# Kernel optimization log

Measured on AMD Instinct MI355X. Metric: run time of the kernel, lower is better.

## Reference

```python
import jax, jax.numpy as jnp
import numpy as np

B, L, XS, YS, A, C, NL = 32, 4096, 256, 256, 4, 64, 5  # batch, seq, x_size, y_size, n_actions, hid_cnn, cnn_layers


def _conv2d(x, w):
    # x: [N,Cin,H,W], w: [Cout,Cin,3,3], stride 1, pad 1 ('SAME')
    return jax.lax.conv_general_dilated(x, w, (1, 1), 'SAME',
                                        dimension_numbers=('NCHW', 'OIHW', 'NCHW'))


def setup_inputs() -> dict:
    key = jax.random.key(0)
    ks = jax.random.split(key, 16)
    stdv = 1.0 / np.sqrt(XS)
    inp = {
        'x': jax.random.normal(ks[0], (B, L, XS), jnp.float32),
        'y': jax.random.normal(ks[1], (B, YS), jnp.float32),
        'x_mask': jax.random.randint(ks[2], (B, L), 0, 2) == 1,
        'actions': jax.random.randint(ks[3], (B,), 0, A),
        'weight': jax.random.uniform(ks[4], (YS, XS), jnp.float32, -stdv, stdv),
    }
    chans = [(1, C)] + [(C, C)] * (NL - 2) + [(C, 1)]
    for i, (ci, co) in enumerate(chans):
        bound = 1.0 / np.sqrt(ci * 9)
        inp[f'cw{i}'] = jax.random.uniform(ks[5 + 2 * i], (A, co, ci, 3, 3), jnp.float32, -bound, bound)
        inp[f'cb{i}'] = jax.random.uniform(ks[6 + 2 * i], (A, co), jnp.float32, -bound, bound)
    return inp


def reference(x, y, x_mask, actions, weight,
              cw0, cb0, cw1, cb1, cw2, cb2, cw3, cb3, cw4, cb4):
    img = weight[None, None]  # [1,1,YS,XS] -- weight matrix as a 1-channel image

    def per_action(w0, b0, w1, b1, w2, b2, w3, b3, w4, b4):
        out = img
        layers = ((w0, b0), (w1, b1), (w2, b2), (w3, b3), (w4, b4))
        for i, (w, b) in enumerate(layers):
            out = _conv2d(out, w) + b[None, :, None, None]
            if i < NL - 1:
                out = jax.nn.relu(out)
        return out[0, 0]  # [YS,XS]

    # all per-action conv stacks batched via vmap -> [A,YS,XS]
    W_a = jax.vmap(per_action)(cw0, cb0, cw1, cb1, cw2, cb2, cw3, cb3, cw4, cb4)
    # one-hot multiply + sum over actions == select the per-sample action matrix
    Wy = jnp.einsum('bh,bhx->bx', y, W_a[actions])          # [B,XS]
    xWy = jnp.einsum('blx,bx->bl', x, Wy)                   # [B,L]
    xWy = jnp.where(x_mask, -jnp.inf, xWy)
    return jax.nn.softmax(xWy, axis=-1)  # eval-mode output (training uses log_softmax)
```

## Files before the change

kernel.cpp:

```cpp
#include <hip/hip_runtime.h>
#include <cstdint>
#include <cstddef>

typedef __attribute__((ext_vector_type(8))) short bf16x8;
typedef __attribute__((ext_vector_type(4))) float f32x4;
typedef __attribute__((ext_vector_type(4))) int i32x4;

#define MW  18
#define MH  26
#define MPX (MW * MH)
#define MPP 469

#define LW  18
#define LPX (LW * LW)
#define LPP 325

__device__ inline unsigned short cvt_bf16_rne(float f) {
    unsigned u = __builtin_bit_cast(unsigned, f);
    u = (u + 0x7FFFu + ((u >> 16) & 1u)) >> 16;
    return (unsigned short)u;
}

__global__ void prep_kernel(const float* __restrict__ img,
                            const float* __restrict__ cw0,
                            const float* __restrict__ cb0,
                            unsigned short* __restrict__ act,
                            const float* __restrict__ cw1,
                            const float* __restrict__ cw2,
                            const float* __restrict__ cw3,
                            char* __restrict__ apack,
                            const unsigned int* __restrict__ mask,
                            int* __restrict__ flag) {
    int bid = blockIdx.x, tid = threadIdx.x;

    if (bid < 1024) {
        int y = bid & 255, a = bid >> 8, x = tid;
        float p[3][3];
        #pragma unroll
        for (int ty = 0; ty < 3; ++ty)
            #pragma unroll
            for (int tx = 0; tx < 3; ++tx) {
                int py = y + ty - 1, px = x + tx - 1;
                p[ty][tx] = ((unsigned)py < 256u && (unsigned)px < 256u)
                            ? img[py * 256 + px] : 0.0f;
            }
        const float* w = cw0 + (size_t)a * 64 * 9;
        const float* b = cb0 + a * 64;
        unsigned pk[32];
        #pragma unroll
        for (int co = 0; co < 64; ++co) {
            const float* wc = w + co * 9;
            float acc = b[co];
            #pragma unroll
            for (int ty = 0; ty < 3; ++ty)
                #pragma unroll
                for (int tx = 0; tx < 3; ++tx)
                    acc = fmaf(wc[ty * 3 + tx], p[ty][tx], acc);
            acc = fmaxf(acc, 0.0f);
            unsigned short hv = cvt_bf16_rne(acc);
            if (co & 1) pk[co >> 1] |= ((unsigned)hv << 16);
            else        pk[co >> 1] = (unsigned)hv;
        }
        char* ob = (char*)act + (((size_t)(a << 16) + (y << 8) + x) << 7);
        #pragma unroll
        for (int k = 0; k < 8; ++k)
            *(i32x4*)(ob + k * 16) = *(i32x4*)&pk[k * 4];
        return;
    }

    if (bid < 1240) {
        int idx = (bid - 1024) * 256 + tid;
        int layer = idx / 18432;
        int r = idx - layer * 18432;
        int lane = r & 63, mf = (r >> 6) & 3;
        int t = r >> 8;
        int tap = t % 9, t2 = t / 9;
        int ks = t2 & 1, a = t2 >> 1;
        int n = lane & 15, q = lane >> 4;
        int co = mf * 16 + n;
        int ci0 = ks * 32 + q * 8;
        const float* cw = (layer == 0) ? cw1 : (layer == 1) ? cw2 : cw3;
        unsigned d[4];
        #pragma unroll
        for (int jj = 0; jj < 4; ++jj) {
            unsigned short h0 = cvt_bf16_rne(cw[((size_t)(a * 64 + co) * 64 + ci0 + 2 * jj + 0) * 9 + tap]);
            unsigned short h1 = cvt_bf16_rne(cw[((size_t)(a * 64 + co) * 64 + ci0 + 2 * jj + 1) * 9 + tap]);
            d[jj] = (unsigned)h0 | ((unsigned)h1 << 16);
        }
        *(i32x4*)(apack + (size_t)idx * 16) = *(i32x4*)d;
        return;
    }

    __shared__ int red;
    if (tid == 0) red = 0;
    __syncthreads();
    int f = 0;
    for (int k = 0; k < 128; ++k) {
        unsigned v = mask[k * 256 + tid];
        if (v == 0x3F800000u) f |= 2;
        else if (v > 1u) f |= 1;
    }
    if (f) atomicOr(&red, f);
    __syncthreads();
    if (tid == 0) *flag = red;
}

__global__ __launch_bounds__(256, 2)
void conv_mid_mfma(const unsigned short* __restrict__ act_in,
                   const char* __restrict__ apack_l,
                   const float* __restrict__ cb,
                   unsigned short* __restrict__ act_out) {
    __shared__ i32x4 lds4[8 * MPP];
    int tid = threadIdx.x;
    int a = blockIdx.z;
    int r0 = blockIdx.y * 24, c0 = blockIdx.x * 16;
    const char* actb = (const char*)act_in;

    for (int s = tid; s < 8 * MPX; s += 256) {
        int o = s & 7, px = s >> 3;
        int prow = px / MW, pcol = px - prow * MW;
        int grow = r0 - 1 + prow, gcol = c0 - 1 + pcol;
        i32x4 v = {0, 0, 0, 0};
        if ((unsigned)grow < 256u && (unsigned)gcol < 256u)
            v = *(const i32x4*)(actb + (((size_t)(a << 16) + (grow << 8) + gcol) << 7) + (o << 4));
        lds4[o * MPP + px] = v;
    }
    __syncthreads();

    int lane = tid & 63, wv = tid >> 6;
    int n = lane & 15, q = lane >> 4;
    int rbase = wv * 6;

    f32x4 acc[4][6];
    #pragma unroll
    for (int mf = 0; mf < 4; ++mf) {
        f32x4 bb = *(const f32x4*)(cb + a * 64 + mf * 16 + q * 4);
        #pragma unroll
        for (int nf = 0; nf < 6; ++nf) acc[mf][nf] = bb;
    }

    const char* ap = apack_l + (size_t)a * 73728 + lane * 16;
    const i32x4* bbase = lds4 + q * MPP + rbase * MW + n;

    #pragma unroll
    for (int ks = 0; ks < 2; ++ks) {
        const char* apk = ap + ks * 36864;
        const i32x4* bks = bbase + ks * 4 * MPP;
        #pragma unroll
        for (int tap = 0; tap < 9; ++tap) {
            const int ty = tap / 3, tx = tap - ty * 3;
            bf16x8 Af[4], Bf[6];
            #pragma unroll
            for (int mf = 0; mf < 4; ++mf)
                Af[mf] = __builtin_bit_cast(bf16x8,
                    *(const i32x4*)(apk + tap * 4096 + mf * 1024));
            #pragma unroll
            for (int nf = 0; nf < 6; ++nf)
                Bf[nf] = __builtin_bit_cast(bf16x8, bks[(nf + ty) * MW + tx]);
            #pragma unroll
            for (int mf = 0; mf < 4; ++mf)
                #pragma unroll
                for (int nf = 0; nf < 6; ++nf)
                    acc[mf][nf] = __builtin_amdgcn_mfma_f32_16x16x32_bf16(
                        Af[mf], Bf[nf], acc[mf][nf], 0, 0, 0);
        }
    }

    #pragma unroll
    for (int nf = 0; nf < 6; ++nf) {
        int grow = r0 + rbase + nf;
        if (grow < 256) {
            int gcol = c0 + n;
            char* ob = (char*)act_out + (((size_t)(a << 16) + (grow << 8) + gcol) << 7) + q * 8;
            #pragma unroll
            for (int mf = 0; mf < 4; ++mf) {
                f32x4 v = acc[mf][nf];
                unsigned d0 = (unsigned)cvt_bf16_rne(fmaxf(v.x, 0.0f))
                            | ((unsigned)cvt_bf16_rne(fmaxf(v.y, 0.0f)) << 16);
                unsigned d1 = (unsigned)cvt_bf16_rne(fmaxf(v.z, 0.0f))
                            | ((unsigned)cvt_bf16_rne(fmaxf(v.w, 0.0f)) << 16);
                uint2 st; st.x = d0; st.y = d1;
                *(uint2*)(ob + mf * 32) = st;
            }
        }
    }
}

__global__ __launch_bounds__(256, 3)
void conv_last_kernel(const unsigned short* __restrict__ act,
                      const float* __restrict__ cw4,
                      const float* __restrict__ cb4,
                      float* __restrict__ W_a) {
    __shared__ i32x4 lds4[8 * LPP];
    int tid = threadIdx.x;
    int a = blockIdx.z;
    int r0 = blockIdx.y * 16, c0 = blockIdx.x * 16;
    const char* actb = (const char*)act;

    for (int s = tid; s < 8 * LPX; s += 256) {
        int o = s & 7, px = s >> 3;
        int prow = px / LW, pcol = px - prow * LW;
        int grow = r0 - 1 + prow, gcol = c0 - 1 + pcol;
        i32x4 v = {0, 0, 0, 0};
        if ((unsigned)grow < 256u && (unsigned)gcol < 256u)
            v = *(const i32x4*)(actb + (((size_t)(a << 16) + (grow << 8) + gcol) << 7) + (o << 4));
        lds4[o * LPP + px] = v;
    }
    __syncthreads();

    int lane = tid & 63, wv = tid >> 6;
    int o = lane & 7, pl = lane >> 3;

    float wr[8][9];
    #pragma unroll
    for (int j = 0; j < 8; ++j) {
        const float* wp = cw4 + ((size_t)a * 64 + o * 8 + j) * 9;
        #pragma unroll
        for (int t = 0; t < 9; ++t) wr[j][t] = wp[t];
    }
    float bias = cb4[a];
    const i32x4* lbase = lds4 + o * LPP;

    #pragma unroll
    for (int i = 0; i < 8; ++i) {
        int r = 2 * i + (wv >> 1);
        int c = ((wv & 1) << 3) + pl;
        float p = 0.0f;
        #pragma unroll
        for (int ty = 0; ty < 3; ++ty)
            #pragma unroll
            for (int tx = 0; tx < 3; ++tx) {
                i32x4 v = lbase[(r + ty) * LW + (c + tx)];
                const unsigned* dv = (const unsigned*)&v;
                #pragma unroll
                for (int k = 0; k < 4; ++k) {
                    unsigned d = dv[k];
                    float flo = __builtin_bit_cast(float, d << 16);
                    float fhi = __builtin_bit_cast(float, d & 0xFFFF0000u);
                    p = fmaf(flo, wr[2 * k + 0][ty * 3 + tx], p);
                    p = fmaf(fhi, wr[2 * k + 1][ty * 3 + tx], p);
                }
            }
        p += __shfl_xor(p, 1, 64);
        p += __shfl_xor(p, 2, 64);
        p += __shfl_xor(p, 4, 64);
        if (o == 0)
            W_a[(size_t)(a << 16) + ((r0 + r) << 8) + (c0 + c)] = p + bias;
    }
}

__global__ void wy_kernel(const float* __restrict__ yv,
                          const int* __restrict__ actions,
                          const float* __restrict__ W_a,
                          float* __restrict__ Wy) {
    int b = blockIdx.x, x = threadIdx.x;
    int a = actions[b];
    const float* Wp = W_a + (size_t)a * 65536;
    const float* yb = yv + b * 256;
    float acc = 0.0f;
    #pragma unroll 8
    for (int h = 0; h < 256; ++h)
        acc = fmaf(yb[h], Wp[(size_t)h * 256 + x], acc);
    Wy[b * 256 + x] = acc;
}

__global__ void logits_kernel(const float* __restrict__ xv,
                              const void* __restrict__ mask,
                              const int* __restrict__ flag,
                              const float* __restrict__ Wy,
                              float* __restrict__ out) {
    int tid = threadIdx.x, lane = tid & 63, wave = tid >> 6;
    int b = blockIdx.y;
    int fl = *flag;
    float4 wy4 = *(const float4*)(Wy + b * 256 + lane * 4);
    const float* xb = xv + (size_t)b * 4096 * 256;
    int l0 = blockIdx.x * 128 + wave * 32;
    for (int li = 0; li < 32; ++li) {
        int l = l0 + li;
        const float4 x4 = *(const float4*)(xb + (size_t)l * 256 + lane * 4);
        float p = x4.x * wy4.x + x4.y * wy4.y + x4.z * wy4.z + x4.w * wy4.w;
        #pragma unroll
        for (int off = 32; off > 0; off >>= 1)
            p += __shfl_xor(p, off, 64);
        if (lane == 0) {
            size_t mi = (size_t)b * 4096 + l;
            bool msk;
            if (fl & 2)      msk = ((const float*)mask)[mi] != 0.0f;
            else if (fl & 1) msk = ((const unsigned char*)mask)[mi] != 0;
            else             msk = ((const int*)mask)[mi] != 0;
            out[mi] = msk ? -__builtin_inff() : p;
        }
    }
}

__global__ void softmax_kernel(float* __restrict__ out) {
    int b = blockIdx.x, tid = threadIdx.x;
    int lane = tid & 63, wid = tid >> 6;
    float* row = out + (size_t)b * 4096;
    float v[4];
    float m = -__builtin_inff();
    #pragma unroll
    for (int i = 0; i < 4; ++i) { v[i] = row[tid + i * 1024]; m = fmaxf(m, v[i]); }
    #pragma unroll
    for (int off = 32; off > 0; off >>= 1) m = fmaxf(m, __shfl_xor(m, off, 64));
    __shared__ float redm[16];
    __shared__ float reds[16];
    if (lane == 0) redm[wid] = m;
    __syncthreads();
    float M = redm[0];
    #pragma unroll
    for (int j = 1; j < 16; ++j) M = fmaxf(M, redm[j]);
    float s = 0.0f;
    #pragma unroll
    for (int i = 0; i < 4; ++i) { v[i] = expf(v[i] - M); s += v[i]; }
    #pragma unroll
    for (int off = 32; off > 0; off >>= 1) s += __shfl_xor(s, off, 64);
    if (lane == 0) reds[wid] = s;
    __syncthreads();
    float S = 0.0f;
    #pragma unroll
    for (int j = 0; j < 16; ++j) S += reds[j];
    float inv = 1.0f / S;
    #pragma unroll
    for (int i = 0; i < 4; ++i) row[tid + i * 1024] = v[i] * inv;
}

extern "C" void kernel_launch(void* const* d_in, const int* in_sizes, int n_in,
                              void* d_out, int out_size, void* d_ws, size_t ws_size,
                              hipStream_t stream) {
    const float* xv      = (const float*)d_in[0];
    const float* yv      = (const float*)d_in[1];
    const void*  xmask   = d_in[2];
    const int*   actions = (const int*)d_in[3];
    const float* weight  = (const float*)d_in[4];
    const float* cw0 = (const float*)d_in[5];
    const float* cb0 = (const float*)d_in[6];
    const float* cw1 = (const float*)d_in[7];
    const float* cb1 = (const float*)d_in[8];
    const float* cw2 = (const float*)d_in[9];
    const float* cb2 = (const float*)d_in[10];
    const float* cw3 = (const float*)d_in[11];
    const float* cb3 = (const float*)d_in[12];
    const float* cw4 = (const float*)d_in[13];
    const float* cb4 = (const float*)d_in[14];
    float* out = (float*)d_out;

    char* ws = (char*)d_ws;
    unsigned short* bufA = (unsigned short*)ws;
    unsigned short* bufB = (unsigned short*)(ws + 33554432);
    char*  apack = ws + 67108864;
    float* W_a   = (float*)(ws + 67993600);
    float* Wy    = (float*)(ws + 69042176);
    int*   flag  = (int*)(ws + 69074944);

    prep_kernel<<<1241, 256, 0, stream>>>(weight, cw0, cb0, bufA,
                                          cw1, cw2, cw3, apack,
                                          (const unsigned int*)xmask, flag);

    conv_mid_mfma<<<dim3(16, 11, 4), 256, 0, stream>>>(bufA, apack,          cb1, bufB);
    conv_mid_mfma<<<dim3(16, 11, 4), 256, 0, stream>>>(bufB, apack + 294912, cb2, bufA);
    conv_mid_mfma<<<dim3(16, 11, 4), 256, 0, stream>>>(bufA, apack + 589824, cb3, bufB);
    conv_last_kernel<<<dim3(16, 16, 4), 256, 0, stream>>>(bufB, cw4, cb4, W_a);

    wy_kernel<<<32, 256, 0, stream>>>(yv, actions, W_a, Wy);
    logits_kernel<<<dim3(32, 32), 256, 0, stream>>>(xv, xmask, flag, Wy, out);
    softmax_kernel<<<32, 1024, 0, stream>>>(out);
}
```

Baseline: 406.7 us.

## Fuse all stages into one persistent kernel with global atomic barriers

Replaces the sequence of eight kernel launches with a single persistent 512-block kernel that runs prep, three MFMA conv layers, the last conv, Wy/logits and softmax, separated by software grid barriers built on agent-scope atomics. The mid conv tiles grow to 32x16 and stage the input channels into LDS in two halves to cut shared memory use, and the Wy product is recomputed per block instead of going through a separate kernel. This is meant to remove launch gaps and tail effects between stages. In exchange it relies on all 512 blocks being co-resident (2 per CU) to avoid deadlock, adds barrier spin cost, computes Wy redundantly 16 times per batch, and runs softmax on only 32 blocks.

```diff
diff --git a/kernel.cpp b/kernel.cpp
--- a/kernel.cpp
+++ b/kernel.cpp
@@ -6,14 +6,20 @@
 typedef __attribute__((ext_vector_type(4))) float f32x4;
 typedef __attribute__((ext_vector_type(4))) int i32x4;
 
-#define MW  18
-#define MH  26
-#define MPX (MW * MH)
-#define MPP 469
-
-#define LW  18
+#define NB 512
+
+#define TR 32
+#define TC 16
+#define HR 34
+#define HC 18
+#define HPX (HR * HC)
+#define HPP 613
+
+#define LW 18
 #define LPX (LW * LW)
 #define LPP 325
+
+#define SH_BYTES 41600
 
 __device__ inline unsigned short cvt_bf16_rne(float f) {
     unsigned u = __builtin_bit_cast(unsigned, f);
@@ -21,20 +27,122 @@
     return (unsigned short)u;
 }
 
-__global__ void prep_kernel(const float* __restrict__ img,
-                            const float* __restrict__ cw0,
-                            const float* __restrict__ cb0,
-                            unsigned short* __restrict__ act,
-                            const float* __restrict__ cw1,
-                            const float* __restrict__ cw2,
-                            const float* __restrict__ cw3,
-                            char* __restrict__ apack,
-                            const unsigned int* __restrict__ mask,
-                            int* __restrict__ flag) {
-    int bid = blockIdx.x, tid = threadIdx.x;
-
-    if (bid < 1024) {
-        int y = bid & 255, a = bid >> 8, x = tid;
+__global__ void init_kernel(int* bar) {
+    if (threadIdx.x < 16) bar[threadIdx.x] = 0;
+}
+
+__device__ inline void gbar(int* bar, int idx) {
+    __syncthreads();
+    if (threadIdx.x == 0) {
+        __hip_atomic_fetch_add(bar + idx, 1, __ATOMIC_ACQ_REL, __HIP_MEMORY_SCOPE_AGENT);
+        while (__hip_atomic_load(bar + idx, __ATOMIC_ACQUIRE, __HIP_MEMORY_SCOPE_AGENT) < NB)
+            __builtin_amdgcn_s_sleep(1);
+    }
+    __syncthreads();
+}
+
+__device__ inline void mid_layer(const char* __restrict__ actb,
+                                 const char* __restrict__ apl,
+                                 const float* __restrict__ cb,
+                                 char* __restrict__ outb,
+                                 int wg, int tid, i32x4* lds) {
+    int a = wg >> 7;
+    int idx = wg & 127;
+    int r0 = (idx >> 4) * TR;
+    int c0 = (idx & 15) * TC;
+    int lane = tid & 63, wv = tid >> 6;
+    int n = lane & 15, q = lane >> 4;
+    int rbase = wv * 8;
+
+    f32x4 acc[4][8];
+    #pragma unroll
+    for (int mf = 0; mf < 4; ++mf) {
+        f32x4 bb = *(const f32x4*)(cb + a * 64 + mf * 16 + q * 4);
+        #pragma unroll
+        for (int nf = 0; nf < 8; ++nf) acc[mf][nf] = bb;
+    }
+
+    const char* ap = apl + (size_t)a * 73728 + lane * 16;
+    const i32x4* bb0 = lds + q * HPP + rbase * HC + n;
+
+    for (int ks = 0; ks < 2; ++ks) {
+        __syncthreads();
+        for (int s = tid; s < 4 * HPX; s += 256) {
+            int o = s & 3, px = s >> 2;
+            int prow = px / HC, pcol = px - prow * HC;
+            int grow = r0 - 1 + prow, gcol = c0 - 1 + pcol;
+            i32x4 v = {0, 0, 0, 0};
+            if ((unsigned)grow < 256u && (unsigned)gcol < 256u)
+                v = *(const i32x4*)(actb + (((size_t)((a << 16) + (grow << 8) + gcol)) << 7)
+                                    + ks * 64 + (o << 4));
+            lds[o * HPP + px] = v;
+        }
+        __syncthreads();
+
+        const char* apk = ap + ks * 36864;
+        #pragma unroll
+        for (int tap = 0; tap < 9; ++tap) {
+            const int ty = tap / 3, tx = tap - ty * 3;
+            bf16x8 Af[4], Bf[8];
+            #pragma unroll
+            for (int mf = 0; mf < 4; ++mf)
+                Af[mf] = __builtin_bit_cast(bf16x8,
+                    *(const i32x4*)(apk + tap * 4096 + mf * 1024));
+            #pragma unroll
+            for (int nf = 0; nf < 8; ++nf)
+                Bf[nf] = __builtin_bit_cast(bf16x8, bb0[(nf + ty) * HC + tx]);
+            #pragma unroll
+            for (int mf = 0; mf < 4; ++mf)
+                #pragma unroll
+                for (int nf = 0; nf < 8; ++nf)
+                    acc[mf][nf] = __builtin_amdgcn_mfma_f32_16x16x32_bf16(
+                        Af[mf], Bf[nf], acc[mf][nf], 0, 0, 0);
+        }
+    }
+
+    #pragma unroll
+    for (int nf = 0; nf < 8; ++nf) {
+        int grow = r0 + rbase + nf;
+        int gcol = c0 + n;
+        char* ob = outb + (((size_t)((a << 16) + (grow << 8) + gcol)) << 7) + q * 8;
+        #pragma unroll
+        for (int mf = 0; mf < 4; ++mf) {
+            f32x4 v = acc[mf][nf];
+            unsigned d0 = (unsigned)cvt_bf16_rne(fmaxf(v.x, 0.0f))
+                        | ((unsigned)cvt_bf16_rne(fmaxf(v.y, 0.0f)) << 16);
+            unsigned d1 = (unsigned)cvt_bf16_rne(fmaxf(v.z, 0.0f))
+                        | ((unsigned)cvt_bf16_rne(fmaxf(v.w, 0.0f)) << 16);
+            uint2 st; st.x = d0; st.y = d1;
+            *(uint2*)(ob + mf * 32) = st;
+        }
+    }
+}
+
+__global__ __launch_bounds__(256, 2)
+void mega_kernel(const float* __restrict__ xv,
+                 const float* __restrict__ yv,
+                 const void*  __restrict__ xmask,
+                 const int*   __restrict__ actions,
+                 const float* __restrict__ weight,
+                 const float* __restrict__ cw0, const float* __restrict__ cb0,
+                 const float* __restrict__ cw1, const float* __restrict__ cb1,
+                 const float* __restrict__ cw2, const float* __restrict__ cb2,
+                 const float* __restrict__ cw3, const float* __restrict__ cb3,
+                 const float* __restrict__ cw4, const float* __restrict__ cb4,
+                 float* __restrict__ out,
+                 unsigned short* __restrict__ bufA,
+                 unsigned short* __restrict__ bufB,
+                 char* __restrict__ apack,
+                 float* __restrict__ W_a,
+                 int* __restrict__ flag,
+                 int* __restrict__ bar) {
+    __shared__ char shraw[SH_BYTES] __attribute__((aligned(16)));
+    i32x4* lds = (i32x4*)shraw;
+    int wg = blockIdx.x, tid = threadIdx.x;
+
+    for (int j = 0; j < 2; ++j) {
+        int job = wg * 2 + j;
+        int a = job >> 8, y = job & 255, x = tid;
         float p[3][3];
         #pragma unroll
         for (int ty = 0; ty < 3; ++ty)
@@ -42,7 +150,7 @@
             for (int tx = 0; tx < 3; ++tx) {
                 int py = y + ty - 1, px = x + tx - 1;
                 p[ty][tx] = ((unsigned)py < 256u && (unsigned)px < 256u)
-                            ? img[py * 256 + px] : 0.0f;
+                            ? weight[py * 256 + px] : 0.0f;
             }
         const float* w = cw0 + (size_t)a * 64 * 9;
         const float* b = cb0 + a * 64;
@@ -61,268 +169,180 @@
             if (co & 1) pk[co >> 1] |= ((unsigned)hv << 16);
             else        pk[co >> 1] = (unsigned)hv;
         }
-        char* ob = (char*)act + (((size_t)(a << 16) + (y << 8) + x) << 7);
+        char* ob = (char*)bufA + (((size_t)((a << 16) + (y << 8) + x)) << 7);
         #pragma unroll
         for (int k = 0; k < 8; ++k)
             *(i32x4*)(ob + k * 16) = *(i32x4*)&pk[k * 4];
-        return;
-    }
-
-    if (bid < 1240) {
-        int idx = (bid - 1024) * 256 + tid;
-        int layer = idx / 18432;
-        int r = idx - layer * 18432;
-        int lane = r & 63, mf = (r >> 6) & 3;
-        int t = r >> 8;
-        int tap = t % 9, t2 = t / 9;
-        int ks = t2 & 1, a = t2 >> 1;
-        int n = lane & 15, q = lane >> 4;
-        int co = mf * 16 + n;
-        int ci0 = ks * 32 + q * 8;
-        const float* cw = (layer == 0) ? cw1 : (layer == 1) ? cw2 : cw3;
-        unsigned d[4];
-        #pragma unroll
-        for (int jj = 0; jj < 4; ++jj) {
-            unsigned short h0 = cvt_bf16_rne(cw[((size_t)(a * 64 + co) * 64 + ci0 + 2 * jj + 0) * 9 + tap]);
-            unsigned short h1 = cvt_bf16_rne(cw[((size_t)(a * 64 + co) * 64 + ci0 + 2 * jj + 1) * 9 + tap]);
-            d[jj] = (unsigned)h0 | ((unsigned)h1 << 16);
-        }
-        *(i32x4*)(apack + (size_t)idx * 16) = *(i32x4*)d;
-        return;
-    }
-
-    __shared__ int red;
-    if (tid == 0) red = 0;
-    __syncthreads();
-    int f = 0;
-    for (int k = 0; k < 128; ++k) {
-        unsigned v = mask[k * 256 + tid];
-        if (v == 0x3F800000u) f |= 2;
-        else if (v > 1u) f |= 1;
-    }
-    if (f) atomicOr(&red, f);
-    __syncthreads();
-    if (tid == 0) *flag = red;
-}
-
-__global__ __launch_bounds__(256, 2)
-void conv_mid_mfma(const unsigned short* __restrict__ act_in,
-                   const char* __restrict__ apack_l,
-                   const float* __restrict__ cb,
-                   unsigned short* __restrict__ act_out) {
-    __shared__ i32x4 lds4[8 * MPP];
-    int tid = threadIdx.x;
-    int a = blockIdx.z;
-    int r0 = blockIdx.y * 24, c0 = blockIdx.x * 16;
-    const char* actb = (const char*)act_in;
-
-    for (int s = tid; s < 8 * MPX; s += 256) {
-        int o = s & 7, px = s >> 3;
-        int prow = px / MW, pcol = px - prow * MW;
-        int grow = r0 - 1 + prow, gcol = c0 - 1 + pcol;
-        i32x4 v = {0, 0, 0, 0};
-        if ((unsigned)grow < 256u && (unsigned)gcol < 256u)
-            v = *(const i32x4*)(actb + (((size_t)(a << 16) + (grow << 8) + gcol) << 7) + (o << 4));
-        lds4[o * MPP + px] = v;
-    }
-    __syncthreads();
-
-    int lane = tid & 63, wv = tid >> 6;
-    int n = lane & 15, q = lane >> 4;
-    int rbase = wv * 6;
-
-    f32x4 acc[4][6];
-    #pragma unroll
-    for (int mf = 0; mf < 4; ++mf) {
-        f32x4 bb = *(const f32x4*)(cb + a * 64 + mf * 16 + q * 4);
-        #pragma unroll
-        for (int nf = 0; nf < 6; ++nf) acc[mf][nf] = bb;
-    }
-
-    const char* ap = apack_l + (size_t)a * 73728 + lane * 16;
-    const i32x4* bbase = lds4 + q * MPP + rbase * MW + n;
-
-    #pragma unroll
-    for (int ks = 0; ks < 2; ++ks) {
-        const char* apk = ap + ks * 36864;
-        const i32x4* bks = bbase + ks * 4 * MPP;
-        #pragma unroll
-        for (int tap = 0; tap < 9; ++tap) {
-            const int ty = tap / 3, tx = tap - ty * 3;
-            bf16x8 Af[4], Bf[6];
-            #pragma unroll
-            for (int mf = 0; mf < 4; ++mf)
-                Af[mf] = __builtin_bit_cast(bf16x8,
-                    *(const i32x4*)(apk + tap * 4096 + mf * 1024));
-            #pragma unroll
-            for (int nf = 0; nf < 6; ++nf)
-                Bf[nf] = __builtin_bit_cast(bf16x8, bks[(nf + ty) * MW + tx]);
-            #pragma unroll
-            for (int mf = 0; mf < 4; ++mf)
+    }
+
+    {
+        int i = wg * 256 + tid;
+        if (i < 55296) {
+            int layer = i / 18432;
+            int r = i - layer * 18432;
+            int lane = r & 63, mf = (r >> 6) & 3;
+            int t = r >> 8;
+            int tap = t % 9, t2 = t / 9;
+            int ks = t2 & 1, a = t2 >> 1;
+            int nn = lane & 15, qq = lane >> 4;
+            int co = mf * 16 + nn;
+            int ci0 = ks * 32 + qq * 8;
+            const float* cw = (layer == 0) ? cw1 : (layer == 1) ? cw2 : cw3;
+            unsigned d[4];
+            #pragma unroll
+            for (int jj = 0; jj < 4; ++jj) {
+                unsigned short h0 = cvt_bf16_rne(cw[((size_t)(a * 64 + co) * 64 + ci0 + 2 * jj + 0) * 9 + tap]);
+                unsigned short h1 = cvt_bf16_rne(cw[((size_t)(a * 64 + co) * 64 + ci0 + 2 * jj + 1) * 9 + tap]);
+                d[jj] = (unsigned)h0 | ((unsigned)h1 << 16);
+            }
+            *(i32x4*)(apack + (size_t)i * 16) = *(i32x4*)d;
+        }
+    }
+
+    if (wg == 511) {
+        int* red = (int*)shraw;
+        if (tid == 0) *red = 0;
+        __syncthreads();
+        const unsigned* m = (const unsigned*)xmask;
+        int f = 0;
+        for (int k = 0; k < 128; ++k) {
+            unsigned v = m[k * 256 + tid];
+            if (v == 0x3F800000u) f |= 2;
+            else if (v > 1u) f |= 1;
+        }
+        if (f) atomicOr(red, f);
+        __syncthreads();
+        if (tid == 0) *flag = *red;
+    }
+    gbar(bar, 0);
+
+    mid_layer((const char*)bufA, apack,          cb1, (char*)bufB, wg, tid, lds);
+    gbar(bar, 1);
+    mid_layer((const char*)bufB, apack + 294912, cb2, (char*)bufA, wg, tid, lds);
+    gbar(bar, 2);
+    mid_layer((const char*)bufA, apack + 589824, cb3, (char*)bufB, wg, tid, lds);
+    gbar(bar, 3);
+
+    for (int j = 0; j < 2; ++j) {
+        int job = wg * 2 + j;
+        int a = job >> 8;
+        int idx = job & 255;
+        int r0 = (idx >> 4) * 16, c0 = (idx & 15) * 16;
+        __syncthreads();
+        for (int s = tid; s < 8 * LPX; s += 256) {
+            int o = s & 7, px = s >> 3;
+            int prow = px / LW, pcol = px - prow * LW;
+            int grow = r0 - 1 + prow, gcol = c0 - 1 + pcol;
+            i32x4 v = {0, 0, 0, 0};
+            if ((unsigned)grow < 256u && (unsigned)gcol < 256u)
+                v = *(const i32x4*)((const char*)bufB +
+                    (((size_t)((a << 16) + (grow << 8) + gcol)) << 7) + (o << 4));
+            lds[o * LPP + px] = v;
+        }
+        __syncthreads();
+
+        int lane = tid & 63, wv = tid >> 6;
+        int o = lane & 7, pl = lane >> 3;
+        float wr[8][9];
+        #pragma unroll
+        for (int jj = 0; jj < 8; ++jj) {
+            const float* wp = cw4 + ((size_t)a * 64 + o * 8 + jj) * 9;
+            #pragma unroll
+            for (int t = 0; t < 9; ++t) wr[jj][t] = wp[t];
+        }
+        float bias = cb4[a];
+        const i32x4* lbase = lds + o * LPP;
+        #pragma unroll
+        for (int i = 0; i < 8; ++i) {
+            int r = 2 * i + (wv >> 1);
+            int c = ((wv & 1) << 3) + pl;
+            float p = 0.0f;
+            #pragma unroll
+            for (int ty = 0; ty < 3; ++ty)
                 #pragma unroll
-                for (int nf = 0; nf < 6; ++nf)
-                    acc[mf][nf] = __builtin_amdgcn_mfma_f32_16x16x32_bf16(
-                        Af[mf], Bf[nf], acc[mf][nf], 0, 0, 0);
-        }
-    }
-
-    #pragma unroll
-    for (int nf = 0; nf < 6; ++nf) {
-        int grow = r0 + rbase + nf;
-        if (grow < 256) {
-            int gcol = c0 + n;
-            char* ob = (char*)act_out + (((size_t)(a << 16) + (grow << 8) + gcol) << 7) + q * 8;
-            #pragma unroll
-            for (int mf = 0; mf < 4; ++mf) {
-                f32x4 v = acc[mf][nf];
-                unsigned d0 = (unsigned)cvt_bf16_rne(fmaxf(v.x, 0.0f))
-                            | ((unsigned)cvt_bf16_rne(fmaxf(v.y, 0.0f)) << 16);
-                unsigned d1 = (unsigned)cvt_bf16_rne(fmaxf(v.z, 0.0f))
-                            | ((unsigned)cvt_bf16_rne(fmaxf(v.w, 0.0f)) << 16);
-                uint2 st; st.x = d0; st.y = d1;
-                *(uint2*)(ob + mf * 32) = st;
+                for (int tx = 0; tx < 3; ++tx) {
+                    i32x4 v = lbase[(r + ty) * LW + (c + tx)];
+                    const unsigned* dv = (const unsigned*)&v;
+                    #pragma unroll
+                    for (int k = 0; k < 4; ++k) {
+                        unsigned d = dv[k];
+                        float flo = __builtin_bit_cast(float, d << 16);
+                        float fhi = __builtin_bit_cast(float, d & 0xFFFF0000u);
+                        p = fmaf(flo, wr[2 * k + 0][ty * 3 + tx], p);
+                        p = fmaf(fhi, wr[2 * k + 1][ty * 3 + tx], p);
+                    }
+                }
+            p += __shfl_xor(p, 1, 64);
+            p += __shfl_xor(p, 2, 64);
+            p += __shfl_xor(p, 4, 64);
+            if (o == 0)
+                W_a[(size_t)((a << 16) + ((r0 + r) << 8) + (c0 + c))] = p + bias;
+        }
+    }
+    gbar(bar, 4);
+
+    {
+        int b = wg >> 4, seg = wg & 15;
+        int aact = actions[b];
+        const float* yb = yv + b * 256;
+        const float* Wp = W_a + (size_t)aact * 65536;
+        float accw = 0.0f;
+        #pragma unroll 8
+        for (int h = 0; h < 256; ++h)
+            accw = fmaf(yb[h], Wp[h * 256 + tid], accw);
+        float* wyf = (float*)shraw;
+        wyf[tid] = accw;
+        __syncthreads();
+
+        int lane = tid & 63, wv = tid >> 6;
+        int fl = *flag;
+        float4 wy4 = *(const float4*)(wyf + lane * 4);
+        const float* xb = xv + (size_t)b * 4096 * 256;
+        int lb = seg * 256 + wv * 64;
+        for (int it = 0; it < 64; ++it) {
+            int l = lb + it;
+            const float4 x4 = *(const float4*)(xb + (size_t)l * 256 + lane * 4);
+            float p = x4.x * wy4.x + x4.y * wy4.y + x4.z * wy4.z + x4.w * wy4.w;
+            #pragma unroll
+            for (int off = 32; off > 0; off >>= 1)
+                p += __shfl_xor(p, off, 64);
+            if (lane == 0) {
+                size_t mi = (size_t)b * 4096 + l;
+                bool msk;
+                if (fl & 2)      msk = ((const float*)xmask)[mi] != 0.0f;
+                else if (fl & 1) msk = ((const unsigned char*)xmask)[mi] != 0;
+                else             msk = ((const int*)xmask)[mi] != 0;
+                out[mi] = msk ? -__builtin_inff() : p;
             }
         }
     }
-}
-
-__global__ __launch_bounds__(256, 3)
-void conv_last_kernel(const unsigned short* __restrict__ act,
-                      const float* __restrict__ cw4,
-                      const float* __restrict__ cb4,
-                      float* __restrict__ W_a) {
-    __shared__ i32x4 lds4[8 * LPP];
-    int tid = threadIdx.x;
-    int a = blockIdx.z;
-    int r0 = blockIdx.y * 16, c0 = blockIdx.x * 16;
-    const char* actb = (const char*)act;
-
-    for (int s = tid; s < 8 * LPX; s += 256) {
-        int o = s & 7, px = s >> 3;
-        int prow = px / LW, pcol = px - prow * LW;
-        int grow = r0 - 1 + prow, gcol = c0 - 1 + pcol;
-        i32x4 v = {0, 0, 0, 0};
-        if ((unsigned)grow < 256u && (unsigned)gcol < 256u)
-            v = *(const i32x4*)(actb + (((size_t)(a << 16) + (grow << 8) + gcol) << 7) + (o << 4));
-        lds4[o * LPP + px] = v;
-    }
-    __syncthreads();
-
-    int lane = tid & 63, wv = tid >> 6;
-    int o = lane & 7, pl = lane >> 3;
-
-    float wr[8][9];
-    #pragma unroll
-    for (int j = 0; j < 8; ++j) {
-        const float* wp = cw4 + ((size_t)a * 64 + o * 8 + j) * 9;
-        #pragma unroll
-        for (int t = 0; t < 9; ++t) wr[j][t] = wp[t];
-    }
-    float bias = cb4[a];
-    const i32x4* lbase = lds4 + o * LPP;
-
-    #pragma unroll
-    for (int i = 0; i < 8; ++i) {
-        int r = 2 * i + (wv >> 1);
-        int c = ((wv & 1) << 3) + pl;
-        float p = 0.0f;
-        #pragma unroll
-        for (int ty = 0; ty < 3; ++ty)
-            #pragma unroll
-            for (int tx = 0; tx < 3; ++tx) {
-                i32x4 v = lbase[(r + ty) * LW + (c + tx)];
-                const unsigned* dv = (const unsigned*)&v;
-                #pragma unroll
-                for (int k = 0; k < 4; ++k) {
-                    unsigned d = dv[k];
-                    float flo = __builtin_bit_cast(float, d << 16);
-                    float fhi = __builtin_bit_cast(float, d & 0xFFFF0000u);
-                    p = fmaf(flo, wr[2 * k + 0][ty * 3 + tx], p);
-                    p = fmaf(fhi, wr[2 * k + 1][ty * 3 + tx], p);
-                }
-            }
-        p += __shfl_xor(p, 1, 64);
-        p += __shfl_xor(p, 2, 64);
-        p += __shfl_xor(p, 4, 64);
-        if (o == 0)
-            W_a[(size_t)(a << 16) + ((r0 + r) << 8) + (c0 + c)] = p + bias;
-    }
-}
-
-__global__ void wy_kernel(const float* __restrict__ yv,
-                          const int* __restrict__ actions,
-                          const float* __restrict__ W_a,
-                          float* __restrict__ Wy) {
-    int b = blockIdx.x, x = threadIdx.x;
-    int a = actions[b];
-    const float* Wp = W_a + (size_t)a * 65536;
-    const float* yb = yv + b * 256;
-    float acc = 0.0f;
-    #pragma unroll 8
-    for (int h = 0; h < 256; ++h)
-        acc = fmaf(yb[h], Wp[(size_t)h * 256 + x], acc);
-    Wy[b * 256 + x] = acc;
-}
-
-__global__ void logits_kernel(const float* __restrict__ xv,
-                              const void* __restrict__ mask,
-                              const int* __restrict__ flag,
-                              const float* __restrict__ Wy,
-                              float* __restrict__ out) {
-    int tid = threadIdx.x, lane = tid & 63, wave = tid >> 6;
-    int b = blockIdx.y;
-    int fl = *flag;
-    float4 wy4 = *(const float4*)(Wy + b * 256 + lane * 4);
-    const float* xb = xv + (size_t)b * 4096 * 256;
-    int l0 = blockIdx.x * 128 + wave * 32;
-    for (int li = 0; li < 32; ++li) {
-        int l = l0 + li;
-        const float4 x4 = *(const float4*)(xb + (size_t)l * 256 + lane * 4);
-        float p = x4.x * wy4.x + x4.y * wy4.y + x4.z * wy4.z + x4.w * wy4.w;
-        #pragma unroll
-        for (int off = 32; off > 0; off >>= 1)
-            p += __shfl_xor(p, off, 64);
-        if (lane == 0) {
-            size_t mi = (size_t)b * 4096 + l;
-            bool msk;
-            if (fl & 2)      msk = ((const float*)mask)[mi] != 0.0f;
-            else if (fl & 1) msk = ((const unsigned char*)mask)[mi] != 0;
-            else             msk = ((const int*)mask)[mi] != 0;
-            out[mi] = msk ? -__builtin_inff() : p;
-        }
-    }
-}
-
-__global__ void softmax_kernel(float* __restrict__ out) {
-    int b = blockIdx.x, tid = threadIdx.x;
-    int lane = tid & 63, wid = tid >> 6;
-    float* row = out + (size_t)b * 4096;
-    float v[4];
-    float m = -__builtin_inff();
-    #pragma unroll
-    for (int i = 0; i < 4; ++i) { v[i] = row[tid + i * 1024]; m = fmaxf(m, v[i]); }
-    #pragma unroll
-    for (int off = 32; off > 0; off >>= 1) m = fmaxf(m, __shfl_xor(m, off, 64));
-    __shared__ float redm[16];
-    __shared__ float reds[16];
-    if (lane == 0) redm[wid] = m;
-    __syncthreads();
-    float M = redm[0];
-    #pragma unroll
-    for (int j = 1; j < 16; ++j) M = fmaxf(M, redm[j]);
-    float s = 0.0f;
-    #pragma unroll
-    for (int i = 0; i < 4; ++i) { v[i] = expf(v[i] - M); s += v[i]; }
-    #pragma unroll
-    for (int off = 32; off > 0; off >>= 1) s += __shfl_xor(s, off, 64);
-    if (lane == 0) reds[wid] = s;
-    __syncthreads();
-    float S = 0.0f;
-    #pragma unroll
-    for (int j = 0; j < 16; ++j) S += reds[j];
-    float inv = 1.0f / S;
-    #pragma unroll
-    for (int i = 0; i < 4; ++i) row[tid + i * 1024] = v[i] * inv;
+    gbar(bar, 5);
+
+    if (wg < 32) {
+        float* row = out + (size_t)wg * 4096;
+        float* sred = (float*)shraw;
+        int lane = tid & 63, wid = tid >> 6;
+        float v[16];
+        float m = -__builtin_inff();
+        #pragma unroll
+        for (int i = 0; i < 16; ++i) { v[i] = row[tid + i * 256]; m = fmaxf(m, v[i]); }
+        #pragma unroll
+        for (int off = 32; off > 0; off >>= 1) m = fmaxf(m, __shfl_xor(m, off, 64));
+        if (lane == 0) sred[wid] = m;
+        __syncthreads();
+        float M = fmaxf(fmaxf(sred[0], sred[1]), fmaxf(sred[2], sred[3]));
+        float s = 0.0f;
+        #pragma unroll
+        for (int i = 0; i < 16; ++i) { v[i] = expf(v[i] - M); s += v[i]; }
+        #pragma unroll
+        for (int off = 32; off > 0; off >>= 1) s += __shfl_xor(s, off, 64);
+        if (lane == 0) sred[8 + wid] = s;
+        __syncthreads();
+        float S = sred[8] + sred[9] + sred[10] + sred[11];
+        float inv = 1.0f / S;
+        #pragma unroll
+        for (int i = 0; i < 16; ++i) row[tid + i * 256] = v[i] * inv;
+    }
 }
 
 extern "C" void kernel_launch(void* const* d_in, const int* in_sizes, int n_in,
@@ -350,19 +370,12 @@
     unsigned short* bufB = (unsigned short*)(ws + 33554432);
     char*  apack = ws + 67108864;
     float* W_a   = (float*)(ws + 67993600);
-    float* Wy    = (float*)(ws + 69042176);
-    int*   flag  = (int*)(ws + 69074944);
-
-    prep_kernel<<<1241, 256, 0, stream>>>(weight, cw0, cb0, bufA,
-                                          cw1, cw2, cw3, apack,
-                                          (const unsigned int*)xmask, flag);
-
-    conv_mid_mfma<<<dim3(16, 11, 4), 256, 0, stream>>>(bufA, apack,          cb1, bufB);
-    conv_mid_mfma<<<dim3(16, 11, 4), 256, 0, stream>>>(bufB, apack + 294912, cb2, bufA);
-    conv_mid_mfma<<<dim3(16, 11, 4), 256, 0, stream>>>(bufA, apack + 589824, cb3, bufB);
-    conv_last_kernel<<<dim3(16, 16, 4), 256, 0, stream>>>(bufB, cw4, cb4, W_a);
-
-    wy_kernel<<<32, 256, 0, stream>>>(yv, actions, W_a, Wy);
-    logits_kernel<<<dim3(32, 32), 256, 0, stream>>>(xv, xmask, flag, Wy, out);
-    softmax_kernel<<<32, 1024, 0, stream>>>(out);
-}
+    int*   flag  = (int*)(ws + 69042176);
+    int*   bar   = (int*)(ws + 69042240);
+
+    init_kernel<<<1, 64, 0, stream>>>(bar);
+    mega_kernel<<<NB, 256, 0, stream>>>(xv, yv, xmask, actions, weight,
+                                        cw0, cb0, cw1, cb1, cw2, cb2,
+                                        cw3, cb3, cw4, cb4,
+                                        out, bufA, bufB, apack, W_a, flag, bar);
+}
```

After: 878.5 us. 116% more time.

## Shrink conv tiles to 16x16 with split-K LDS staging; fuse Wy into logits

Applied to the files above, without the earlier changes.

The mid conv layers now use 16x16 output tiles instead of 24x16 and stage only half the input channels in LDS at a time, looping over two K halves. This cuts the LDS footprint and the accumulator registers, and the launch bound rises from 2 to 4 blocks per CU, so more blocks can be resident. The cost is an extra sync and reload per K half and more halo overhead per output. Separately, the Wy reduction is folded into the logits kernel: each of the 16 blocks per batch row recomputes Wy into shared memory, which removes one launch and the Wy buffer but repeats the 256x256 matvec in every block.

```diff
diff --git a/kernel.cpp b/kernel.cpp
--- a/kernel.cpp
+++ b/kernel.cpp
@@ -6,10 +6,9 @@
 typedef __attribute__((ext_vector_type(4))) float f32x4;
 typedef __attribute__((ext_vector_type(4))) int i32x4;
 
-#define MW  18
-#define MH  26
-#define MPX (MW * MH)
-#define MPP 469
+#define MW   18
+#define MPX  (MW * MW)
+#define MPP  330
 
 #define LW  18
 #define LPX (LW * LW)
@@ -61,7 +60,7 @@
             if (co & 1) pk[co >> 1] |= ((unsigned)hv << 16);
             else        pk[co >> 1] = (unsigned)hv;
         }
-        char* ob = (char*)act + (((size_t)(a << 16) + (y << 8) + x) << 7);
+        char* ob = (char*)act + (((size_t)((a << 16) + (y << 8) + x)) << 7);
         #pragma unroll
         for (int k = 0; k < 8; ++k)
             *(i32x4*)(ob + k * 16) = *(i32x4*)&pk[k * 4];
@@ -105,83 +104,81 @@
     if (tid == 0) *flag = red;
 }
 
-__global__ __launch_bounds__(256, 2)
+__global__ __launch_bounds__(256, 4)
 void conv_mid_mfma(const unsigned short* __restrict__ act_in,
                    const char* __restrict__ apack_l,
                    const float* __restrict__ cb,
                    unsigned short* __restrict__ act_out) {
-    __shared__ i32x4 lds4[8 * MPP];
+    __shared__ i32x4 lds4[4 * MPP];
     int tid = threadIdx.x;
     int a = blockIdx.z;
-    int r0 = blockIdx.y * 24, c0 = blockIdx.x * 16;
+    int r0 = blockIdx.y * 16, c0 = blockIdx.x * 16;
     const char* actb = (const char*)act_in;
-
-    for (int s = tid; s < 8 * MPX; s += 256) {
-        int o = s & 7, px = s >> 3;
-        int prow = px / MW, pcol = px - prow * MW;
-        int grow = r0 - 1 + prow, gcol = c0 - 1 + pcol;
-        i32x4 v = {0, 0, 0, 0};
-        if ((unsigned)grow < 256u && (unsigned)gcol < 256u)
-            v = *(const i32x4*)(actb + (((size_t)(a << 16) + (grow << 8) + gcol) << 7) + (o << 4));
-        lds4[o * MPP + px] = v;
-    }
-    __syncthreads();
 
     int lane = tid & 63, wv = tid >> 6;
     int n = lane & 15, q = lane >> 4;
-    int rbase = wv * 6;
-
-    f32x4 acc[4][6];
+    int rbase = wv * 4;
+
+    f32x4 acc[4][4];
     #pragma unroll
     for (int mf = 0; mf < 4; ++mf) {
         f32x4 bb = *(const f32x4*)(cb + a * 64 + mf * 16 + q * 4);
         #pragma unroll
-        for (int nf = 0; nf < 6; ++nf) acc[mf][nf] = bb;
+        for (int nf = 0; nf < 4; ++nf) acc[mf][nf] = bb;
     }
 
     const char* ap = apack_l + (size_t)a * 73728 + lane * 16;
-    const i32x4* bbase = lds4 + q * MPP + rbase * MW + n;
-
-    #pragma unroll
+    const i32x4* bb0 = lds4 + q * MPP + rbase * MW + n;
+
     for (int ks = 0; ks < 2; ++ks) {
+        __syncthreads();
+        for (int s = tid; s < 4 * MPX; s += 256) {
+            int o = s & 3, px = s >> 2;
+            int prow = px / MW, pcol = px - prow * MW;
+            int grow = r0 - 1 + prow, gcol = c0 - 1 + pcol;
+            i32x4 v = {0, 0, 0, 0};
+            if ((unsigned)grow < 256u && (unsigned)gcol < 256u)
+                v = *(const i32x4*)(actb + (((size_t)((a << 16) + (grow << 8) + gcol)) << 7)
+                                    + ks * 64 + (o << 4));
+            lds4[o * MPP + px] = v;
+        }
+        __syncthreads();
+
         const char* apk = ap + ks * 36864;
-        const i32x4* bks = bbase + ks * 4 * MPP;
         #pragma unroll
         for (int tap = 0; tap < 9; ++tap) {
             const int ty = tap / 3, tx = tap - ty * 3;
-            bf16x8 Af[4], Bf[6];
+            bf16x8 Af[4], Bf[4];
             #pragma unroll
             for (int mf = 0; mf < 4; ++mf)
                 Af[mf] = __builtin_bit_cast(bf16x8,
                     *(const i32x4*)(apk + tap * 4096 + mf * 1024));
             #pragma unroll
-            for (int nf = 0; nf < 6; ++nf)
-                Bf[nf] = __builtin_bit_cast(bf16x8, bks[(nf + ty) * MW + tx]);
+            for (int nf = 0; nf < 4; ++nf)
+                Bf[nf] = __builtin_bit_cast(bf16x8, bb0[(nf + ty) * MW + tx]);
             #pragma unroll
             for (int mf = 0; mf < 4; ++mf)
                 #pragma unroll
-                for (int nf = 0; nf < 6; ++nf)
+                for (int nf = 0; nf < 4; ++nf)
                     acc[mf][nf] = __builtin_amdgcn_mfma_f32_16x16x32_bf16(
                         Af[mf], Bf[nf], acc[mf][nf], 0, 0, 0);
         }
     }
 
     #pragma unroll
-    for (int nf = 0; nf < 6; ++nf) {
+    for (int nf = 0; nf < 4; ++nf) {
         int grow = r0 + rbase + nf;
-        if (grow < 256) {
-            int gcol = c0 + n;
-            char* ob = (char*)act_out + (((size_t)(a << 16) + (grow << 8) + gcol) << 7) + q * 8;
-            #pragma unroll
-            for (int mf = 0; mf < 4; ++mf) {
-                f32x4 v = acc[mf][nf];
-                unsigned d0 = (unsigned)cvt_bf16_rne(fmaxf(v.x, 0.0f))
-                            | ((unsigned)cvt_bf16_rne(fmaxf(v.y, 0.0f)) << 16);
-                unsigned d1 = (unsigned)cvt_bf16_rne(fmaxf(v.z, 0.0f))
-                            | ((unsigned)cvt_bf16_rne(fmaxf(v.w, 0.0f)) << 16);
-                uint2 st; st.x = d0; st.y = d1;
-                *(uint2*)(ob + mf * 32) = st;
-            }
+        int gcol = c0 + n;
+        char* ob = (char*)act_out + (((size_t)((a << 16) + (grow << 8) + gcol)) << 7) + q * 8;
+        #pragma unroll
+        for (int mf = 0; mf < 4; ++mf) {
+            f32x4 v = acc[mf][nf];
+            unsigned d0 = (unsigned)cvt_bf16_rne(fmaxf(v.x, 0.0f))
+                        | ((unsigned)cvt_bf16_rne(fmaxf(v.y, 0.0f)) << 16);
+            unsigned d1 = (unsigned)cvt_bf16_rne(fmaxf(v.z, 0.0f))
+                        | ((unsigned)cvt_bf16_rne(fmaxf(v.w, 0.0f)) << 16);
+            uint2 st; st.x = d0; st.y = d1;
+            *(uint2*)(ob + mf * 32) = st;
         }
     }
 }
@@ -203,7 +200,7 @@
         int grow = r0 - 1 + prow, gcol = c0 - 1 + pcol;
         i32x4 v = {0, 0, 0, 0};
         if ((unsigned)grow < 256u && (unsigned)gcol < 256u)
-            v = *(const i32x4*)(actb + (((size_t)(a << 16) + (grow << 8) + gcol) << 7) + (o << 4));
+            v = *(const i32x4*)(actb + (((size_t)((a << 16) + (grow << 8) + gcol)) << 7) + (o << 4));
         lds4[o * LPP + px] = v;
     }
     __syncthreads();
@@ -245,38 +242,37 @@
         p += __shfl_xor(p, 2, 64);
         p += __shfl_xor(p, 4, 64);
         if (o == 0)
-            W_a[(size_t)(a << 16) + ((r0 + r) << 8) + (c0 + c)] = p + bias;
-    }
-}
-
-__global__ void wy_kernel(const float* __restrict__ yv,
-                          const int* __restrict__ actions,
-                          const float* __restrict__ W_a,
-                          float* __restrict__ Wy) {
-    int b = blockIdx.x, x = threadIdx.x;
-    int a = actions[b];
-    const float* Wp = W_a + (size_t)a * 65536;
+            W_a[(size_t)((a << 16) + ((r0 + r) << 8) + (c0 + c))] = p + bias;
+    }
+}
+
+__global__ void wy_logits_kernel(const float* __restrict__ xv,
+                                 const float* __restrict__ yv,
+                                 const void* __restrict__ xmask,
+                                 const int* __restrict__ actions,
+                                 const float* __restrict__ W_a,
+                                 const int* __restrict__ flag,
+                                 float* __restrict__ out) {
+    __shared__ float wyf[256];
+    int tid = threadIdx.x;
+    int b = blockIdx.y, seg = blockIdx.x;
+    int aact = actions[b];
+    const float* Wp = W_a + (size_t)aact * 65536;
     const float* yb = yv + b * 256;
-    float acc = 0.0f;
+    float accw = 0.0f;
     #pragma unroll 8
     for (int h = 0; h < 256; ++h)
-        acc = fmaf(yb[h], Wp[(size_t)h * 256 + x], acc);
-    Wy[b * 256 + x] = acc;
-}
-
-__global__ void logits_kernel(const float* __restrict__ xv,
-                              const void* __restrict__ mask,
-                              const int* __restrict__ flag,
-                              const float* __restrict__ Wy,
-                              float* __restrict__ out) {
-    int tid = threadIdx.x, lane = tid & 63, wave = tid >> 6;
-    int b = blockIdx.y;
+        accw = fmaf(yb[h], Wp[h * 256 + tid], accw);
+    wyf[tid] = accw;
+    __syncthreads();
+
+    int lane = tid & 63, wv = tid >> 6;
     int fl = *flag;
-    float4 wy4 = *(const float4*)(Wy + b * 256 + lane * 4);
+    float4 wy4 = *(const float4*)(wyf + lane * 4);
     const float* xb = xv + (size_t)b * 4096 * 256;
-    int l0 = blockIdx.x * 128 + wave * 32;
-    for (int li = 0; li < 32; ++li) {
-        int l = l0 + li;
+    int lb = seg * 256 + wv * 64;
+    for (int it = 0; it < 64; ++it) {
+        int l = lb + it;
         const float4 x4 = *(const float4*)(xb + (size_t)l * 256 + lane * 4);
         float p = x4.x * wy4.x + x4.y * wy4.y + x4.z * wy4.z + x4.w * wy4.w;
         #pragma unroll
@@ -285,9 +281,9 @@
         if (lane == 0) {
             size_t mi = (size_t)b * 4096 + l;
             bool msk;
-            if (fl & 2)      msk = ((const float*)mask)[mi] != 0.0f;
-            else if (fl & 1) msk = ((const unsigned char*)mask)[mi] != 0;
-            else             msk = ((const int*)mask)[mi] != 0;
+            if (fl & 2)      msk = ((const float*)xmask)[mi] != 0.0f;
+            else if (fl & 1) msk = ((const unsigned char*)xmask)[mi] != 0;
+            else             msk = ((const int*)xmask)[mi] != 0;
             out[mi] = msk ? -__builtin_inff() : p;
         }
     }
@@ -350,19 +346,18 @@
     unsigned short* bufB = (unsigned short*)(ws + 33554432);
     char*  apack = ws + 67108864;
     float* W_a   = (float*)(ws + 67993600);
-    float* Wy    = (float*)(ws + 69042176);
-    int*   flag  = (int*)(ws + 69074944);
+    int*   flag  = (int*)(ws + 69042176);
 
     prep_kernel<<<1241, 256, 0, stream>>>(weight, cw0, cb0, bufA,
                                           cw1, cw2, cw3, apack,
                                           (const unsigned int*)xmask, flag);
 
-    conv_mid_mfma<<<dim3(16, 11, 4), 256, 0, stream>>>(bufA, apack,          cb1, bufB);
-    conv_mid_mfma<<<dim3(16, 11, 4), 256, 0, stream>>>(bufB, apack + 294912, cb2, bufA);
-    conv_mid_mfma<<<dim3(16, 11, 4), 256, 0, stream>>>(bufA, apack + 589824, cb3, bufB);
+    conv_mid_mfma<<<dim3(16, 16, 4), 256, 0, stream>>>(bufA, apack,          cb1, bufB);
+    conv_mid_mfma<<<dim3(16, 16, 4), 256, 0, stream>>>(bufB, apack + 294912, cb2, bufA);
+    conv_mid_mfma<<<dim3(16, 16, 4), 256, 0, stream>>>(bufA, apack + 589824, cb3, bufB);
     conv_last_kernel<<<dim3(16, 16, 4), 256, 0, stream>>>(bufB, cw4, cb4, W_a);
 
-    wy_kernel<<<32, 256, 0, stream>>>(yv, actions, W_a, Wy);
-    logits_kernel<<<dim3(32, 32), 256, 0, stream>>>(xv, xmask, flag, Wy, out);
+    wy_logits_kernel<<<dim3(16, 32), 256, 0, stream>>>(xv, yv, xmask, actions,
+                                                       W_a, flag, out);
     softmax_kernel<<<32, 1024, 0, stream>>>(out);
 }
```

New measurement: 488.3 us. 1.2x slower.
